# Kernel optimization log

Measured on AMD Instinct MI355X. Metric: run time of the kernel, lower is better.

The kernel has to match this reference:

```python
import jax, jax.numpy as jnp
import numpy as np

B, C, L = 1024, 256, 16   # nodes, channels (num_features), num_ell (dim of 0e+1o+2e+3o)
E = 10                    # num_elements
K3, K2, K1 = 23, 4, 1     # U-matrix path counts for correlation orders 3,2,1


def setup_inputs() -> dict:
    key = jax.random.key(0)
    ks = jax.random.split(key, 8)
    return {
        "x": jax.random.normal(ks[0], (B, C, L), jnp.float32),
        "y": jax.random.normal(ks[1], (B, E), jnp.float32),
        # U buffers (generalized Clebsch-Gordan, here random stand-ins of the right shapes)
        "U3": jax.random.normal(ks[2], (L, L, L, K3), jnp.float32),
        "U2": jax.random.normal(ks[3], (L, L, K2), jnp.float32),
        "U1": jax.random.normal(ks[4], (L, K1), jnp.float32),
        # per-element weights, scaled by 1/num_params as in the module
        "W3": jax.random.normal(ks[5], (E, K3, C), jnp.float32) / K3,
        "W2": jax.random.normal(ks[6], (E, K2, C), jnp.float32) / K2,
        "W1": jax.random.normal(ks[7], (E, K1, C), jnp.float32) / K1,
    }


def reference(x, y, U3, U2, U1, W3, W2, W1):
    # symmetric_cp, irrep_out lmax=0 (scalar output), correlation=3.
    # Main (nu=3): out[b,c,w,v] = sum_{i,k,e} U3[w,v,i,k] W3[e,k,c] x[b,c,i] y[b,e]
    # Efficient order: element-select weights, outer-product over (i,k), then one GEMM with U3.
    w3 = jnp.einsum('ekc,be->bkc', W3, y)              # [B,K3,C]
    q = jnp.einsum('bkc,bci->bcik', w3, x)             # [B,C,L,K3]
    out = jnp.einsum('wvik,bcik->bcwv', U3, q)         # [B,C,L,L]
    # nu=2: weighting then feature contraction
    w2 = jnp.einsum('ekc,be->bkc', W2, y)              # [B,K2,C]
    c2 = jnp.einsum('wvk,bkc->bcwv', U2, w2) + out     # [B,C,L,L]
    out = jnp.einsum('bcwi,bci->bcw', c2, x)           # [B,C,L]
    # nu=1
    w1 = jnp.einsum('ekc,be->bkc', W1, y)              # [B,K1,C]
    c1 = jnp.einsum('wk,bkc->bcw', U1, w1) + out       # [B,C,L]
    out = jnp.einsum('bci,bci->bc', c1, x)             # [B,C]
    return out.reshape(out.shape[0], -1)
```

## Files before the change

kernel.cpp:

```cpp
#include <hip/hip_runtime.h>


#define B_   1024
#define C_   256
#define L_   16
#define E_   10
#define K3_  23
#define K2_  4

#define NM3  816
#define NM2  136
#define MTOT 992
#define NCH2 61
#define STSTR 260

using f32x4   = __attribute__((ext_vector_type(4))) float;
using f32x16  = __attribute__((ext_vector_type(16))) float;
using short8v = __attribute__((ext_vector_type(8))) short;

__device__ __host__ __forceinline__ constexpr int tri_(int n) { return n * (n + 1) / 2; }
__device__ __host__ __forceinline__ constexpr int tet_(int n) { return n * (n + 1) * (n + 2) / 6; }

struct MTab { unsigned char a[MTOT], b[MTOT], c[MTOT]; };
constexpr MTab mkMT() {
  MTab t = {};
  int m = 0;
  for (int a = 0; a < 16; a++)
    for (int b = a; b < 16; b++)
      for (int c = b; c < 16; c++) { t.a[m] = a; t.b[m] = b; t.c[m] = c; ++m; }
  for (int a = 0; a < 16; a++)
    for (int b = a; b < 16; b++) { t.a[m] = a; t.b[m] = b; t.c[m] = 16; ++m; }
  for (int a = 0; a < 16; a++) { t.a[m] = a; t.b[m] = 16; t.c[m] = 16; ++m; }
  while (m < MTOT) { t.a[m] = 17; t.b[m] = 17; t.c[m] = 17; ++m; }
  return t;
}
constexpr MTab MT = mkMT();

__global__ void prep_kernel(const float* __restrict__ U3, const float* __restrict__ U2,
                            const float* __restrict__ U1, unsigned short* __restrict__ wsFrag) {
  __shared__ float sRow[16][36];
  const int ch = blockIdx.x;
  const int tid = threadIdx.x;
  if (tid < 16) {
    const int m = ch * 16 + tid;
    for (int i = 0; i < 36; i++) sRow[tid][i] = 0.f;
    if (m < NM3) {
      int ia = 0;
      while (tet_(16) - tet_(16 - (ia + 1)) <= m) ia++;
      int rem = m - (tet_(16) - tet_(16 - ia));
      int ib = ia;
      while (tri_(16 - ia) - tri_(16 - (ib + 1)) <= rem) ib++;
      int ic = ib + (rem - (tri_(16 - ia) - tri_(16 - ib)));
      int pw[6] = {ia, ia, ib, ib, ic, ic};
      int pv[6] = {ib, ic, ia, ic, ia, ib};
      int pi[6] = {ic, ib, ic, ia, ib, ia};
      bool use[6];
      for (int p = 0; p < 6; p++) {
        bool dup = false;
        for (int q = 0; q < p; q++)
          dup = dup || (pw[p] == pw[q] && pv[p] == pv[q] && pi[p] == pi[q]);
        use[p] = !dup;
      }
      for (int k = 0; k < K3_; k++) {
        float s = 0.f;
        for (int p = 0; p < 6; p++)
          if (use[p]) s += U3[((pw[p] * L_ + pv[p]) * L_ + pi[p]) * K3_ + k];
        sRow[tid][k] = s;
      }
    } else if (m < NM3 + NM2) {
      const int pidx = m - NM3;
      int ia = 0;
      while (136 - tri_(16 - (ia + 1)) <= pidx) ia++;
      int ib = ia + (pidx - (136 - tri_(16 - ia)));
      for (int k2 = 0; k2 < K2_; k2++) {
        float s = U2[(ia * L_ + ib) * K2_ + k2];
        if (ia != ib) s += U2[(ib * L_ + ia) * K2_ + k2];
        sRow[tid][23 + k2] = s;
      }
    } else if (m < NM3 + NM2 + L_) {
      sRow[tid][27] = U1[m - NM3 - NM2];
    }
  }
  __syncthreads();
  {
    const int lane = tid & 63, part = tid >> 6;
    unsigned short v16[8];
    for (int j = 0; j < 8; j++) {
      float v = sRow[(lane >> 5) * 8 + j][lane & 31];
      unsigned vb = __float_as_uint(v);
      unsigned short h = (unsigned short)(vb >> 16);
      if (part == 0) {
        v16[j] = h;
      } else {
        float lres = v - __uint_as_float(((unsigned)h) << 16);
        v16[j] = (unsigned short)(__float_as_uint(lres) >> 16);
      }
    }
    unsigned* dst = (unsigned*)(wsFrag + ((size_t)(ch * 2 + part) * 64 + lane) * 8);
    for (int p = 0; p < 4; p++)
      dst[p] = (unsigned)v16[2 * p] | ((unsigned)v16[2 * p + 1] << 16);
  }
}

__device__ __forceinline__ void lane32_swap(unsigned& a, unsigned& b) {
#if defined(__has_builtin) && __has_builtin(__builtin_amdgcn_permlane32_swap)
  auto r = __builtin_amdgcn_permlane32_swap((int)a, (int)b, false, false);
  a = (unsigned)r[0];
  b = (unsigned)r[1];
#else
  asm volatile("v_permlane32_swap_b32 %0, %1" : "+v"(a), "+v"(b));
#endif
}

template <int CH>
__device__ __forceinline__ void chunk_body(
    const float (&XX)[18], const float4* __restrict__ Bg, int lane,
    float4& nbH, float4& nbL, f32x16& acc0, f32x16& acc1) {
  unsigned pk0[4], pk1[4];
  #pragma unroll
  for (int i = 0; i < 4; ++i) {
    {
      const int m0 = CH * 16 + 2 * i;
      float p0 = XX[MT.a[m0]] * XX[MT.b[m0]] * XX[MT.c[m0]];
      float p1 = XX[MT.a[m0 + 1]] * XX[MT.b[m0 + 1]] * XX[MT.c[m0 + 1]];
      asm("v_cvt_pk_bf16_f32 %0, %1, %2" : "=v"(pk0[i]) : "v"(p0), "v"(p1));
    }
    {
      const int m0 = CH * 16 + 8 + 2 * i;
      float p0 = XX[MT.a[m0]] * XX[MT.b[m0]] * XX[MT.c[m0]];
      float p1 = XX[MT.a[m0 + 1]] * XX[MT.b[m0 + 1]] * XX[MT.c[m0 + 1]];
      asm("v_cvt_pk_bf16_f32 %0, %1, %2" : "=v"(pk1[i]) : "v"(p0), "v"(p1));
    }
    lane32_swap(pk0[i], pk1[i]);
  }

  float4 bh = nbH, bl = nbL;
  if constexpr (CH + 1 < NCH2) {
    nbH = Bg[(CH + 1) * 128 + lane];
    nbL = Bg[(CH + 1) * 128 + 64 + lane];
  }
  short8v A0, A1, BH, BL;
  __builtin_memcpy(&A0, pk0, 16);
  __builtin_memcpy(&A1, pk1, 16);
  __builtin_memcpy(&BH, &bh, 16);
  __builtin_memcpy(&BL, &bl, 16);

  acc0 = __builtin_amdgcn_mfma_f32_32x32x16_bf16(A0, BH, acc0, 0, 0, 0);
  acc1 = __builtin_amdgcn_mfma_f32_32x32x16_bf16(A1, BH, acc1, 0, 0, 0);
  acc0 = __builtin_amdgcn_mfma_f32_32x32x16_bf16(A0, BL, acc0, 0, 0, 0);
  acc1 = __builtin_amdgcn_mfma_f32_32x32x16_bf16(A1, BL, acc1, 0, 0, 0);
}

template <int CH>
struct Loop {
  static __device__ __forceinline__ void run(
      const float (&XX)[18], const float4* __restrict__ Bg, int lane,
      float4& nbH, float4& nbL, f32x16& acc0, f32x16& acc1) {
    chunk_body<CH>(XX, Bg, lane, nbH, nbL, acc0, acc1);
    Loop<CH + 1>::run(XX, Bg, lane, nbH, nbL, acc0, acc1);
  }
};
template <>
struct Loop<NCH2> {
  static __device__ __forceinline__ void run(
      const float (&)[18], const float4* __restrict__, int, float4&, float4&,
      f32x16&, f32x16&) {}
};

__global__ __launch_bounds__(256, 2) void symcon_kernel(
    const float* __restrict__ x,
    const float* __restrict__ y,
    const float* __restrict__ W3,
    const float* __restrict__ W2,
    const float* __restrict__ W1,
    const unsigned short* __restrict__ wsFrag,
    float* __restrict__ out)
{
  __shared__ __attribute__((aligned(16))) float sT[28 * STSTR];

  const int tid = threadIdx.x, c = tid, b = blockIdx.x;
  const int lane = tid & 63;
  const int wid = tid >> 6;

  float XX[18];
  {
    const float4* xg = (const float4*)(x + ((size_t)b * C_ + c) * L_);
    #pragma unroll
    for (int i = 0; i < 4; i++) {
      float4 v = xg[i];
      XX[i * 4 + 0] = v.x; XX[i * 4 + 1] = v.y;
      XX[i * 4 + 2] = v.z; XX[i * 4 + 3] = v.w;
    }
    XX[16] = 1.f; XX[17] = 0.f;
  }

  const float4* Bg = (const float4*)wsFrag;
  float4 nbH = Bg[lane], nbL = Bg[64 + lane];
  f32x16 acc0 = (f32x16)0.f, acc1 = (f32x16)0.f;

  Loop<0>::run(XX, Bg, lane, nbH, nbL, acc0, acc1);

  const int kcol = lane & 31, hi = lane >> 5;
  if (kcol < 28) {
    #pragma unroll
    for (int q = 0; q < 4; ++q) {
      f32x4 v0, v1;
      #pragma unroll
      for (int i2 = 0; i2 < 4; ++i2) {
        v0[i2] = acc0[4 * q + i2];
        v1[i2] = acc1[4 * q + i2];
      }
      *(f32x4*)&sT[kcol * STSTR + wid * 64 +      8 * q + 4 * hi] = v0;
      *(f32x4*)&sT[kcol * STSTR + wid * 64 + 32 + 8 * q + 4 * hi] = v1;
    }
  }
  __syncthreads();
  float t[28];
  #pragma unroll
  for (int k = 0; k < 28; ++k) t[k] = sT[k * STSTR + tid];

  float yreg[E_];
  #pragma unroll
  for (int e = 0; e < E_; e++) yreg[e] = y[b * E_ + e];

  float result = 0.f;
  #pragma unroll
  for (int k = 0; k < K3_; k++) {
    const float* w3p = &W3[k * C_ + c];
    float w3k = 0.f;
    #pragma unroll
    for (int e = 0; e < E_; e++) w3k += w3p[e * K3_ * C_] * yreg[e];
    result += t[k] * w3k;
  }
  #pragma unroll
  for (int k2 = 0; k2 < K2_; k2++) {
    const float* w2p = &W2[k2 * C_ + c];
    float w2k = 0.f;
    #pragma unroll
    for (int e = 0; e < E_; e++) w2k += w2p[e * K2_ * C_] * yreg[e];
    result += t[23 + k2] * w2k;
  }
  {
    float w1v = 0.f;
    #pragma unroll
    for (int e = 0; e < E_; e++) w1v += W1[e * C_ + c] * yreg[e];
    result += t[27] * w1v;
  }

  out[(size_t)b * C_ + c] = result;
}

extern "C" void kernel_launch(void* const* d_in, const int* in_sizes, int n_in,
                              void* d_out, int out_size, void* d_ws, size_t ws_size,
                              hipStream_t stream) {
  const float* x  = (const float*)d_in[0];
  const float* y  = (const float*)d_in[1];
  const float* U3 = (const float*)d_in[2];
  const float* U2 = (const float*)d_in[3];
  const float* U1 = (const float*)d_in[4];
  const float* W3 = (const float*)d_in[5];
  const float* W2 = (const float*)d_in[6];
  const float* W1 = (const float*)d_in[7];
  float* out = (float*)d_out;

  unsigned short* wsFrag = (unsigned short*)d_ws;

  prep_kernel<<<dim3(NCH2), dim3(128), 0, stream>>>(U3, U2, U1, wsFrag);
  symcon_kernel<<<dim3(B_), dim3(256), 0, stream>>>(
      x, y, W3, W2, W1, wsFrag, out);
}
```

Measured before the change: 131.0 us.

## Split blocks into single-wave workgroups and deepen B-fragment prefetch to two chunks

Each 256-thread block covering one node becomes four 64-thread single-wave blocks, each covering 64 channels. This removes the block-wide __syncthreads and shrinks the shared transpose buffer per block. The global B-fragment loads are now double-buffered two chunks ahead instead of one, to hide memory latency behind the MFMAs. In exchange it uses more registers for the extra prefetch buffers and launches four times as many blocks. The launch_bounds value of 2 now describes tiny 64-thread blocks, so it may not give the intended occupancy.

```diff
diff --git a/kernel.cpp b/kernel.cpp
--- a/kernel.cpp
+++ b/kernel.cpp
@@ -12,7 +12,7 @@
 #define NM2  136
 #define MTOT 992
 #define NCH2 61
-#define STSTR 260
+#define STSTR 68
 
 using f32x4   = __attribute__((ext_vector_type(4))) float;
 using f32x16  = __attribute__((ext_vector_type(16))) float;
@@ -115,7 +115,8 @@
 template <int CH>
 __device__ __forceinline__ void chunk_body(
     const float (&XX)[18], const float4* __restrict__ Bg, int lane,
-    float4& nbH, float4& nbL, f32x16& acc0, f32x16& acc1) {
+    float4& nbH0, float4& nbL0, float4& nbH1, float4& nbL1,
+    f32x16& acc0, f32x16& acc1) {
   unsigned pk0[4], pk1[4];
   #pragma unroll
   for (int i = 0; i < 4; ++i) {
@@ -134,10 +135,16 @@
     lane32_swap(pk0[i], pk1[i]);
   }
 
-  float4 bh = nbH, bl = nbL;
-  if constexpr (CH + 1 < NCH2) {
-    nbH = Bg[(CH + 1) * 128 + lane];
-    nbL = Bg[(CH + 1) * 128 + 64 + lane];
+  float4 bh, bl;
+  if constexpr ((CH & 1) == 0) { bh = nbH0; bl = nbL0; } else { bh = nbH1; bl = nbL1; }
+  if constexpr (CH + 2 < NCH2) {
+    if constexpr ((CH & 1) == 0) {
+      nbH0 = Bg[(CH + 2) * 128 + lane];
+      nbL0 = Bg[(CH + 2) * 128 + 64 + lane];
+    } else {
+      nbH1 = Bg[(CH + 2) * 128 + lane];
+      nbL1 = Bg[(CH + 2) * 128 + 64 + lane];
+    }
   }
   short8v A0, A1, BH, BL;
   __builtin_memcpy(&A0, pk0, 16);
@@ -155,19 +162,20 @@
 struct Loop {
   static __device__ __forceinline__ void run(
       const float (&XX)[18], const float4* __restrict__ Bg, int lane,
-      float4& nbH, float4& nbL, f32x16& acc0, f32x16& acc1) {
-    chunk_body<CH>(XX, Bg, lane, nbH, nbL, acc0, acc1);
-    Loop<CH + 1>::run(XX, Bg, lane, nbH, nbL, acc0, acc1);
+      float4& nbH0, float4& nbL0, float4& nbH1, float4& nbL1,
+      f32x16& acc0, f32x16& acc1) {
+    chunk_body<CH>(XX, Bg, lane, nbH0, nbL0, nbH1, nbL1, acc0, acc1);
+    Loop<CH + 1>::run(XX, Bg, lane, nbH0, nbL0, nbH1, nbL1, acc0, acc1);
   }
 };
 template <>
 struct Loop<NCH2> {
   static __device__ __forceinline__ void run(
-      const float (&)[18], const float4* __restrict__, int, float4&, float4&,
-      f32x16&, f32x16&) {}
+      const float (&)[18], const float4* __restrict__, int,
+      float4&, float4&, float4&, float4&, f32x16&, f32x16&) {}
 };
 
-__global__ __launch_bounds__(256, 2) void symcon_kernel(
+__global__ __launch_bounds__(64, 2) void symcon_kernel(
     const float* __restrict__ x,
     const float* __restrict__ y,
     const float* __restrict__ W3,
@@ -178,9 +186,10 @@
 {
   __shared__ __attribute__((aligned(16))) float sT[28 * STSTR];
 
-  const int tid = threadIdx.x, c = tid, b = blockIdx.x;
-  const int lane = tid & 63;
-  const int wid = tid >> 6;
+  const int lane = threadIdx.x;
+  const int bb = blockIdx.x;
+  const int b = bb >> 2;
+  const int c = (bb & 3) * 64 + lane;
 
   float XX[18];
   {
@@ -195,10 +204,11 @@
   }
 
   const float4* Bg = (const float4*)wsFrag;
-  float4 nbH = Bg[lane], nbL = Bg[64 + lane];
+  float4 nbH0 = Bg[lane],        nbL0 = Bg[64 + lane];
+  float4 nbH1 = Bg[128 + lane],  nbL1 = Bg[192 + lane];
   f32x16 acc0 = (f32x16)0.f, acc1 = (f32x16)0.f;
 
-  Loop<0>::run(XX, Bg, lane, nbH, nbL, acc0, acc1);
+  Loop<0>::run(XX, Bg, lane, nbH0, nbL0, nbH1, nbL1, acc0, acc1);
 
   const int kcol = lane & 31, hi = lane >> 5;
   if (kcol < 28) {
@@ -210,14 +220,13 @@
         v0[i2] = acc0[4 * q + i2];
         v1[i2] = acc1[4 * q + i2];
       }
-      *(f32x4*)&sT[kcol * STSTR + wid * 64 +      8 * q + 4 * hi] = v0;
-      *(f32x4*)&sT[kcol * STSTR + wid * 64 + 32 + 8 * q + 4 * hi] = v1;
-    }
-  }
-  __syncthreads();
+      *(f32x4*)&sT[kcol * STSTR +      8 * q + 4 * hi] = v0;
+      *(f32x4*)&sT[kcol * STSTR + 32 + 8 * q + 4 * hi] = v1;
+    }
+  }
   float t[28];
   #pragma unroll
-  for (int k = 0; k < 28; ++k) t[k] = sT[k * STSTR + tid];
+  for (int k = 0; k < 28; ++k) t[k] = sT[k * STSTR + lane];
 
   float yreg[E_];
   #pragma unroll
@@ -266,6 +275,6 @@
   unsigned short* wsFrag = (unsigned short*)d_ws;
 
   prep_kernel<<<dim3(NCH2), dim3(128), 0, stream>>>(U3, U2, U1, wsFrag);
-  symcon_kernel<<<dim3(B_), dim3(256), 0, stream>>>(
+  symcon_kernel<<<dim3(B_ * 4), dim3(64), 0, stream>>>(
       x, y, W3, W2, W1, wsFrag, out);
 }
```

New measurement: 129.7 us. No clear change (-1.0%).
